# Kernel optimization log

Measured on AMD Instinct MI355X. Metric: run time of the kernel, lower is better.

Reference implementation:

```python
import jax, jax.numpy as jnp
import numpy as np

# HGIN_classifier: two relational-GIN layers with ReLU between.
# FastRGIN layer math (relational GIN, eps=0, single-linear MLP):
#   agg_r[i] = sum_{(j->i) with edge_type r} x[j]          (per-relation neighbor sum)
#   out[i]   = (1+eps) * x[i] @ W_self + sum_r agg_r[i] @ W_r + b

N = 100000      # nodes
E = 1600000     # edges (avg degree 16)
R = 2           # relations (follower / following)
DIN, DH, DOUT = 128, 256, 2
EPS = 0.0


def setup_inputs() -> dict:
    key = jax.random.key(0)
    ks = jax.random.split(key, 8)
    x = jax.random.normal(ks[0], (N, DIN), dtype=jnp.float32)
    edge_index = jax.random.randint(ks[1], (2, E), 0, N, dtype=jnp.int64)
    edge_type = jax.random.randint(ks[2], (E,), 0, R, dtype=jnp.int64)
    s1 = 1.0 / np.sqrt(DIN).astype(np.float32)
    s2 = 1.0 / np.sqrt(DH).astype(np.float32)
    w1_self = jax.random.normal(ks[3], (DIN, DH), jnp.float32) * s1
    w1_rel = jax.random.normal(ks[4], (R, DIN, DH), jnp.float32) * s1
    b1 = jnp.zeros((DH,), jnp.float32)
    w2_self = jax.random.normal(ks[5], (DH, DOUT), jnp.float32) * s2
    w2_rel = jax.random.normal(ks[6], (R, DH, DOUT), jnp.float32) * s2
    b2 = jnp.zeros((DOUT,), jnp.float32)
    return {"x": x, "edge_index": edge_index, "edge_type": edge_type,
            "w1_self": w1_self, "w1_rel": w1_rel, "b1": b1,
            "w2_self": w2_self, "w2_rel": w2_rel, "b2": b2}


def _rgin_layer(x, src, dst, etype, w_self, w_rel, b):
    n = x.shape[0]
    r = w_rel.shape[0]
    # fused (node, relation) segment id so one segment_sum handles all relations
    seg = dst * r + etype                                   # [E]
    agg = jax.ops.segment_sum(x[src], seg, num_segments=n * r)  # [N*R, d_in]
    agg = agg.reshape(n, r, -1)                              # [N, R, d_in]
    return (1.0 + EPS) * (x @ w_self) + jnp.einsum('nri,rio->no', agg, w_rel) + b


def reference(x, edge_index, edge_type, w1_self, w1_rel, b1, w2_self, w2_rel, b2):
    src, dst = edge_index[0], edge_index[1]
    h = jax.nn.relu(_rgin_layer(x, src, dst, edge_type, w1_self, w1_rel, b1))
    out = _rgin_layer(h, src, dst, edge_type, w2_self, w2_rel, b2)
    return out
```

## Files before the change

kernel.cpp:

```cpp
#include <hip/hip_runtime.h>


typedef _Float16 f16;
typedef _Float16 f16x2 __attribute__((ext_vector_type(2)));
typedef _Float16 f16x4 __attribute__((ext_vector_type(4)));
typedef _Float16 f16x8 __attribute__((ext_vector_type(8)));
typedef float    f32x4 __attribute__((ext_vector_type(4)));

constexpr int NN   = 100000;
constexpr int NR   = NN * 2;
constexpr int NB   = 512;
constexpr int BSH  = 9;
constexpr int CHUNK = 8192;

__global__ void zero_small(int* __restrict__ gcnt) {
  int t = threadIdx.x;
  if (t < NB) gcnt[t] = 0;
}

__global__ void bucketA(const int* __restrict__ dst, const int* __restrict__ et,
                        int* __restrict__ gcnt, int E) {
  __shared__ int h[NB];
  int t = threadIdx.x;
  for (int b = t; b < NB; b += 256) h[b] = 0;
  __syncthreads();
  int lo = blockIdx.x * CHUNK, hi = min(E, lo + CHUNK);
  for (int e = lo + t; e < hi; e += 256)
    atomicAdd(&h[(dst[e] * 2 + et[e]) >> BSH], 1);
  __syncthreads();
  for (int b = t; b < NB; b += 256) {
    int c = h[b];
    if (c) atomicAdd(&gcnt[b], c);
  }
}

__global__ void bscan(const int* __restrict__ gcnt, int* __restrict__ bstart,
                      int* __restrict__ gbase) {
  __shared__ int s[NB];
  int t = threadIdx.x;
  int v = gcnt[t];
  s[t] = v;
  __syncthreads();
  #pragma unroll
  for (int o = 1; o < NB; o <<= 1) {
    int u = (t >= o) ? s[t - o] : 0;
    __syncthreads();
    s[t] += u;
    __syncthreads();
  }
  bstart[t] = s[t] - v;
  gbase[t]  = s[t] - v;
  if (t == NB - 1) bstart[NB] = s[t];
}

__global__ void bucketB(const int* __restrict__ src, const int* __restrict__ dst,
                        const int* __restrict__ et, int* __restrict__ gbase,
                        int2* __restrict__ ebuf, int E) {
  __shared__ int h[NB], base[NB];
  int t = threadIdx.x;
  for (int b = t; b < NB; b += 256) h[b] = 0;
  __syncthreads();
  int lo = blockIdx.x * CHUNK, hi = min(E, lo + CHUNK);
  for (int e = lo + t; e < hi; e += 256)
    atomicAdd(&h[(dst[e] * 2 + et[e]) >> BSH], 1);
  __syncthreads();
  for (int b = t; b < NB; b += 256) {
    int c = h[b];
    base[b] = c ? atomicAdd(&gbase[b], c) : 0;
    h[b] = 0;
  }
  __syncthreads();
  for (int e = lo + t; e < hi; e += 256) {
    int seg = dst[e] * 2 + et[e];
    int b = seg >> BSH;
    int r = atomicAdd(&h[b], 1);
    ebuf[base[b] + r] = make_int2(src[e], seg);
  }
}

__global__ void bucketC(const int2* __restrict__ ebuf, const int* __restrict__ bstart,
                        int* __restrict__ off, int* __restrict__ srcs) {
  __shared__ int sh[NB], soff[NB], cnt[NB], tmp[256];
  int b = blockIdx.x, t = threadIdx.x;
  int lo = bstart[b], hi = bstart[b + 1];
  for (int s0 = t; s0 < NB; s0 += 256) { sh[s0] = 0; cnt[s0] = 0; }
  __syncthreads();
  for (int e = lo + t; e < hi; e += 256)
    atomicAdd(&sh[ebuf[e].y - (b << BSH)], 1);
  __syncthreads();
  int a0 = sh[2 * t], a1 = sh[2 * t + 1];
  tmp[t] = a0 + a1;
  __syncthreads();
  #pragma unroll
  for (int o = 1; o < 256; o <<= 1) {
    int u = (t >= o) ? tmp[t - o] : 0;
    __syncthreads();
    tmp[t] += u;
    __syncthreads();
  }
  int ex = tmp[t] - (a0 + a1);
  soff[2 * t] = ex;
  soff[2 * t + 1] = ex + a0;
  __syncthreads();
  int g0 = (b << BSH) + 2 * t;
  if (g0 <= NR)     off[g0]     = lo + soff[2 * t];
  if (g0 + 1 <= NR) off[g0 + 1] = lo + soff[2 * t + 1];
  for (int e = lo + t; e < hi; e += 256) {
    int2 p = ebuf[e];
    int s = p.y - (b << BSH);
    int r = atomicAdd(&cnt[s], 1);
    srcs[lo + soff[s] + r] = p.x;
  }
}

__global__ void cvt_x(const float4* __restrict__ xf, f16* __restrict__ xh, int n4) {
  int i = blockIdx.x * blockDim.x + threadIdx.x;
  if (i >= n4) return;
  float4 v = xf[i];
  f16x4 h;
  h.x = (f16)v.x; h.y = (f16)v.y; h.z = (f16)v.z; h.w = (f16)v.w;
  *(f16x4*)(xh + (size_t)i * 4) = h;
}

__global__ void cvt_w(const float* __restrict__ w1s, const float* __restrict__ w1r,
                      f16* __restrict__ w1t) {
  int id = blockIdx.x * blockDim.x + threadIdx.x;
  if (id >= 12 * 256 * 32) return;
  int ks = id >> 13, rem = id & 8191;
  int n = rem >> 5, ki = rem & 31;
  int k = ks * 32 + ki;
  float v = (k < 128) ? w1s[k * 256 + n] : w1r[(k - 128) * 256 + n];
  w1t[id] = (f16)v;
}

__global__ void aggregate(const f16* __restrict__ xh, const int* __restrict__ off,
                          const int* __restrict__ srcs, f16* __restrict__ aggh) {
  int w = (blockIdx.x * blockDim.x + threadIdx.x) >> 6;
  if (w >= NN) return;
  int lane = threadIdx.x & 63;
  int e0 = off[2 * w];
  int e1 = off[2 * w + 1];
  int e2 = off[2 * w + 2];
  float a0 = 0.f, a1 = 0.f, c0 = 0.f, c1 = 0.f;
  int e = e0;
  for (; e + 3 < e1; e += 4) {
    f16x2 v0 = *(const f16x2*)(xh + (long)srcs[e] * 128 + lane * 2);
    f16x2 v1 = *(const f16x2*)(xh + (long)srcs[e + 1] * 128 + lane * 2);
    f16x2 v2 = *(const f16x2*)(xh + (long)srcs[e + 2] * 128 + lane * 2);
    f16x2 v3 = *(const f16x2*)(xh + (long)srcs[e + 3] * 128 + lane * 2);
    a0 += (float)v0.x + (float)v1.x + (float)v2.x + (float)v3.x;
    a1 += (float)v0.y + (float)v1.y + (float)v2.y + (float)v3.y;
  }
  for (; e < e1; ++e) {
    f16x2 v = *(const f16x2*)(xh + (long)srcs[e] * 128 + lane * 2);
    a0 += (float)v.x; a1 += (float)v.y;
  }
  e = e1;
  for (; e + 3 < e2; e += 4) {
    f16x2 v0 = *(const f16x2*)(xh + (long)srcs[e] * 128 + lane * 2);
    f16x2 v1 = *(const f16x2*)(xh + (long)srcs[e + 1] * 128 + lane * 2);
    f16x2 v2 = *(const f16x2*)(xh + (long)srcs[e + 2] * 128 + lane * 2);
    f16x2 v3 = *(const f16x2*)(xh + (long)srcs[e + 3] * 128 + lane * 2);
    c0 += (float)v0.x + (float)v1.x + (float)v2.x + (float)v3.x;
    c1 += (float)v0.y + (float)v1.y + (float)v2.y + (float)v3.y;
  }
  for (; e < e2; ++e) {
    f16x2 v = *(const f16x2*)(xh + (long)srcs[e] * 128 + lane * 2);
    c0 += (float)v.x; c1 += (float)v.y;
  }
  f16* row = aggh + (long)w * 256;
  f16x2 o0; o0.x = (f16)a0; o0.y = (f16)a1;
  f16x2 o1; o1.x = (f16)c0; o1.y = (f16)c1;
  *(f16x2*)(row + lane * 2) = o0;
  *(f16x2*)(row + 128 + lane * 2) = o1;
}

__global__ __launch_bounds__(256) void gemm_mfma(
    const f16* __restrict__ xh, const f16* __restrict__ aggh,
    const f16* __restrict__ w1t,
    const float* __restrict__ b1, const float* __restrict__ w2s,
    const float* __restrict__ w2r, const float* __restrict__ b2,
    float* __restrict__ z2, float* __restrict__ out) {
  __shared__ float zbuf[4][64][6];
  const int t = threadIdx.x;
  const int lane = t & 63, wv = t >> 6;
  const int ml = lane & 15, quad = lane >> 4;
  const long rowBase = (long)blockIdx.x * 64;

  long rowc[4];
  #pragma unroll
  for (int mt = 0; mt < 4; ++mt) {
    long r = rowBase + mt * 16 + ml;
    rowc[mt] = r < NN ? r : (NN - 1);
  }
  const f16* bbase = w1t + (long)(wv * 64 + ml) * 32 + quad * 8;

  f32x4 acc[4][4];
  #pragma unroll
  for (int mt = 0; mt < 4; ++mt)
    #pragma unroll
    for (int nt = 0; nt < 4; ++nt) acc[mt][nt] = (f32x4)(0.f);

  #pragma unroll
  for (int ks = 0; ks < 12; ++ks) {
    f16x8 af[4], bf[4];
    #pragma unroll
    for (int mt = 0; mt < 4; ++mt) {
      const f16* ap = (ks < 4)
          ? (xh + rowc[mt] * 128 + ks * 32 + quad * 8)
          : (aggh + rowc[mt] * 256 + (ks - 4) * 32 + quad * 8);
      af[mt] = *(const f16x8*)ap;
    }
    #pragma unroll
    for (int nt = 0; nt < 4; ++nt)
      bf[nt] = *(const f16x8*)(bbase + (long)ks * 8192 + nt * 16 * 32);
    #pragma unroll
    for (int mt = 0; mt < 4; ++mt)
      #pragma unroll
      for (int nt = 0; nt < 4; ++nt)
        acc[mt][nt] = __builtin_amdgcn_mfma_f32_16x16x32_f16(af[mt], bf[nt],
                                                             acc[mt][nt], 0, 0, 0);
  }

  #pragma unroll
  for (int mt = 0; mt < 4; ++mt) {
    float z[4][6];
    #pragma unroll
    for (int rr = 0; rr < 4; ++rr)
      #pragma unroll
      for (int p = 0; p < 6; ++p) z[rr][p] = 0.f;
    #pragma unroll
    for (int nt = 0; nt < 4; ++nt) {
      int col = wv * 64 + nt * 16 + ml;
      float bb = b1[col];
      float wA = w2r[col * 2 + 0];
      float wB = w2r[col * 2 + 1];
      float wC = w2r[512 + col * 2 + 0];
      float wD = w2r[512 + col * 2 + 1];
      float wE = w2s[col * 2 + 0];
      float wF = w2s[col * 2 + 1];
      #pragma unroll
      for (int rr = 0; rr < 4; ++rr) {
        float h = acc[mt][nt][rr] + bb;
        h = h > 0.f ? h : 0.f;
        z[rr][0] = fmaf(h, wA, z[rr][0]);
        z[rr][1] = fmaf(h, wB, z[rr][1]);
        z[rr][2] = fmaf(h, wC, z[rr][2]);
        z[rr][3] = fmaf(h, wD, z[rr][3]);
        z[rr][4] = fmaf(h, wE, z[rr][4]);
        z[rr][5] = fmaf(h, wF, z[rr][5]);
      }
    }
    #pragma unroll
    for (int rr = 0; rr < 4; ++rr)
      #pragma unroll
      for (int p = 0; p < 6; ++p) {
        float v = z[rr][p];
        v += __shfl_xor(v, 1);
        v += __shfl_xor(v, 2);
        v += __shfl_xor(v, 4);
        v += __shfl_xor(v, 8);
        if (ml == 0) zbuf[wv][mt * 16 + quad * 4 + rr][p] = v;
      }
  }
  __syncthreads();
  for (int i = t; i < 384; i += 256) {
    int r = i / 6, p = i % 6;
    long grow = rowBase + r;
    if (grow < NN) {
      float v = zbuf[0][r][p] + zbuf[1][r][p] + zbuf[2][r][p] + zbuf[3][r][p];
      if (p < 4) z2[grow * 4 + p] = v;
      else       out[grow * 2 + (p - 4)] = v + b2[p - 4];
    }
  }
}

__global__ void gather2(const float* __restrict__ z2, const int* __restrict__ off,
                        const int* __restrict__ srcs, float* __restrict__ out) {
  int tid = blockIdx.x * blockDim.x + threadIdx.x;
  int n = tid >> 2;
  if (n >= NN) return;
  int sub = tid & 3;
  int e0 = off[2 * n];
  int e1 = off[2 * n + 1];
  int e2 = off[2 * n + 2];
  float o0 = 0.f, o1 = 0.f;
  for (int e = e0 + sub; e < e1; e += 4) {
    float2 v = *(const float2*)(z2 + (long)srcs[e] * 4);
    o0 += v.x; o1 += v.y;
  }
  for (int e = e1 + sub; e < e2; e += 4) {
    float2 v = *(const float2*)(z2 + (long)srcs[e] * 4 + 2);
    o0 += v.x; o1 += v.y;
  }
  o0 += __shfl_xor(o0, 1); o1 += __shfl_xor(o1, 1);
  o0 += __shfl_xor(o0, 2); o1 += __shfl_xor(o1, 2);
  if (sub == 0) {
    out[n * 2 + 0] += o0;
    out[n * 2 + 1] += o1;
  }
}

extern "C" void kernel_launch(void* const* d_in, const int* in_sizes, int n_in,
                              void* d_out, int out_size, void* d_ws, size_t ws_size,
                              hipStream_t stream) {
  const float* x   = (const float*)d_in[0];
  const int*   ei  = (const int*)d_in[1];
  const int*   et  = (const int*)d_in[2];
  const float* w1s = (const float*)d_in[3];
  const float* w1r = (const float*)d_in[4];
  const float* b1  = (const float*)d_in[5];
  const float* w2s = (const float*)d_in[6];
  const float* w2r = (const float*)d_in[7];
  const float* b2  = (const float*)d_in[8];
  float* out = (float*)d_out;
  const int E = in_sizes[2];
  const int* src = ei;
  const int* dst = ei + E;

  f16*   aggh = (f16*)d_ws;
  f16*   xh   = aggh + (size_t)NN * 256;
  f16*   w1t  = xh + (size_t)NN * 128;
  float* z2   = (float*)(w1t + 12 * 256 * 32);
  int2*  ebuf = (int2*)(z2 + (size_t)NN * 4);
  int*   srcs = (int*)(ebuf + E);
  int*   off  = srcs + E;
  int*   gcnt = off + NR + 1;
  int*   bstart = gcnt + NB;
  int*   gbase  = bstart + NB + 1;

  int nblk = (E + CHUNK - 1) / CHUNK;
  zero_small<<<1, 512, 0, stream>>>(gcnt);
  bucketA<<<nblk, 256, 0, stream>>>(dst, et, gcnt, E);
  bscan<<<1, 512, 0, stream>>>(gcnt, bstart, gbase);
  bucketB<<<nblk, 256, 0, stream>>>(src, dst, et, gbase, ebuf, E);
  bucketC<<<NB, 256, 0, stream>>>(ebuf, bstart, off, srcs);

  int n4 = NN * 128 / 4;
  cvt_x<<<(n4 + 255) / 256, 256, 0, stream>>>((const float4*)x, xh, n4);
  cvt_w<<<(12 * 256 * 32 + 255) / 256, 256, 0, stream>>>(w1s, w1r, w1t);

  aggregate<<<(NN * 64 + 255) / 256, 256, 0, stream>>>(xh, off, srcs, aggh);

  gemm_mfma<<<(NN + 63) / 64, 256, 0, stream>>>(xh, aggh, w1t, b1, w2s, w2r, b2,
                                                z2, out);

  gather2<<<(NN * 4 + 255) / 256, 256, 0, stream>>>(z2, off, srcs, out);
}
```

Before: 385.9 us.

## Fuse neighbor aggregation into layer-1 MFMA GEMM via shared-memory A tile

Removes the separate aggregate kernel and the aggh global buffer. Each GEMM block now stages its 64 rows of xh into padded LDS, runs the per-relation neighbor sums with one wave per node, writes them into the same LDS tile, and then feeds the MFMA loop from LDS. This avoids writing and re-reading the aggregated feature matrix through global memory. In exchange it uses about 50 KB of LDS per block, which limits occupancy, and the gather latency now sits inside the GEMM kernel with only 4 waves per block to hide it.

```diff
diff --git a/kernel.cpp b/kernel.cpp
--- a/kernel.cpp
+++ b/kernel.cpp
@@ -12,6 +12,7 @@
 constexpr int NB   = 512;
 constexpr int BSH  = 9;
 constexpr int CHUNK = 8192;
+constexpr int APAD = 392;
 
 __global__ void zero_small(int* __restrict__ gcnt) {
   int t = threadIdx.x;
@@ -133,68 +134,71 @@
   w1t[id] = (f16)v;
 }
 
-__global__ void aggregate(const f16* __restrict__ xh, const int* __restrict__ off,
-                          const int* __restrict__ srcs, f16* __restrict__ aggh) {
-  int w = (blockIdx.x * blockDim.x + threadIdx.x) >> 6;
-  if (w >= NN) return;
-  int lane = threadIdx.x & 63;
-  int e0 = off[2 * w];
-  int e1 = off[2 * w + 1];
-  int e2 = off[2 * w + 2];
-  float a0 = 0.f, a1 = 0.f, c0 = 0.f, c1 = 0.f;
-  int e = e0;
-  for (; e + 3 < e1; e += 4) {
-    f16x2 v0 = *(const f16x2*)(xh + (long)srcs[e] * 128 + lane * 2);
-    f16x2 v1 = *(const f16x2*)(xh + (long)srcs[e + 1] * 128 + lane * 2);
-    f16x2 v2 = *(const f16x2*)(xh + (long)srcs[e + 2] * 128 + lane * 2);
-    f16x2 v3 = *(const f16x2*)(xh + (long)srcs[e + 3] * 128 + lane * 2);
-    a0 += (float)v0.x + (float)v1.x + (float)v2.x + (float)v3.x;
-    a1 += (float)v0.y + (float)v1.y + (float)v2.y + (float)v3.y;
-  }
-  for (; e < e1; ++e) {
-    f16x2 v = *(const f16x2*)(xh + (long)srcs[e] * 128 + lane * 2);
-    a0 += (float)v.x; a1 += (float)v.y;
-  }
-  e = e1;
-  for (; e + 3 < e2; e += 4) {
-    f16x2 v0 = *(const f16x2*)(xh + (long)srcs[e] * 128 + lane * 2);
-    f16x2 v1 = *(const f16x2*)(xh + (long)srcs[e + 1] * 128 + lane * 2);
-    f16x2 v2 = *(const f16x2*)(xh + (long)srcs[e + 2] * 128 + lane * 2);
-    f16x2 v3 = *(const f16x2*)(xh + (long)srcs[e + 3] * 128 + lane * 2);
-    c0 += (float)v0.x + (float)v1.x + (float)v2.x + (float)v3.x;
-    c1 += (float)v0.y + (float)v1.y + (float)v2.y + (float)v3.y;
-  }
-  for (; e < e2; ++e) {
-    f16x2 v = *(const f16x2*)(xh + (long)srcs[e] * 128 + lane * 2);
-    c0 += (float)v.x; c1 += (float)v.y;
-  }
-  f16* row = aggh + (long)w * 256;
-  f16x2 o0; o0.x = (f16)a0; o0.y = (f16)a1;
-  f16x2 o1; o1.x = (f16)c0; o1.y = (f16)c1;
-  *(f16x2*)(row + lane * 2) = o0;
-  *(f16x2*)(row + 128 + lane * 2) = o1;
-}
-
-__global__ __launch_bounds__(256) void gemm_mfma(
-    const f16* __restrict__ xh, const f16* __restrict__ aggh,
-    const f16* __restrict__ w1t,
+__global__ __launch_bounds__(256) void gemm_fused(
+    const f16* __restrict__ xh, const int* __restrict__ off,
+    const int* __restrict__ srcs, const f16* __restrict__ w1t,
     const float* __restrict__ b1, const float* __restrict__ w2s,
     const float* __restrict__ w2r, const float* __restrict__ b2,
     float* __restrict__ z2, float* __restrict__ out) {
-  __shared__ float zbuf[4][64][6];
+  __shared__ __align__(16) f16 Ash[64 * APAD];
+  float (*zbuf)[64][6] = (float (*)[64][6])(void*)Ash;
   const int t = threadIdx.x;
   const int lane = t & 63, wv = t >> 6;
   const int ml = lane & 15, quad = lane >> 4;
   const long rowBase = (long)blockIdx.x * 64;
 
-  long rowc[4];
-  #pragma unroll
-  for (int mt = 0; mt < 4; ++mt) {
-    long r = rowBase + mt * 16 + ml;
-    rowc[mt] = r < NN ? r : (NN - 1);
-  }
+  #pragma unroll
+  for (int j = 0; j < 4; ++j) {
+    int chunkId = t * 4 + j;
+    int r = chunkId >> 4, c = chunkId & 15;
+    long grow = rowBase + r;
+    uint4 v = make_uint4(0, 0, 0, 0);
+    if (grow < NN) v = *(const uint4*)(xh + grow * 128 + c * 8);
+    *(uint4*)&Ash[r * APAD + c * 8] = v;
+  }
+
+  for (int w = wv; w < 64; w += 4) {
+    long node = rowBase + w;
+    float a0 = 0.f, a1 = 0.f, c0 = 0.f, c1 = 0.f;
+    if (node < NN) {
+      int e0 = off[2 * node], e1 = off[2 * node + 1], e2 = off[2 * node + 2];
+      int e = e0;
+      for (; e + 3 < e1; e += 4) {
+        int s0 = srcs[e], s1 = srcs[e + 1], s2 = srcs[e + 2], s3 = srcs[e + 3];
+        f16x2 v0 = *(const f16x2*)(xh + (long)s0 * 128 + lane * 2);
+        f16x2 v1 = *(const f16x2*)(xh + (long)s1 * 128 + lane * 2);
+        f16x2 v2 = *(const f16x2*)(xh + (long)s2 * 128 + lane * 2);
+        f16x2 v3 = *(const f16x2*)(xh + (long)s3 * 128 + lane * 2);
+        a0 += (float)v0.x + (float)v1.x + (float)v2.x + (float)v3.x;
+        a1 += (float)v0.y + (float)v1.y + (float)v2.y + (float)v3.y;
+      }
+      for (; e < e1; ++e) {
+        f16x2 v = *(const f16x2*)(xh + (long)srcs[e] * 128 + lane * 2);
+        a0 += (float)v.x; a1 += (float)v.y;
+      }
+      e = e1;
+      for (; e + 3 < e2; e += 4) {
+        int s0 = srcs[e], s1 = srcs[e + 1], s2 = srcs[e + 2], s3 = srcs[e + 3];
+        f16x2 v0 = *(const f16x2*)(xh + (long)s0 * 128 + lane * 2);
+        f16x2 v1 = *(const f16x2*)(xh + (long)s1 * 128 + lane * 2);
+        f16x2 v2 = *(const f16x2*)(xh + (long)s2 * 128 + lane * 2);
+        f16x2 v3 = *(const f16x2*)(xh + (long)s3 * 128 + lane * 2);
+        c0 += (float)v0.x + (float)v1.x + (float)v2.x + (float)v3.x;
+        c1 += (float)v0.y + (float)v1.y + (float)v2.y + (float)v3.y;
+      }
+      for (; e < e2; ++e) {
+        f16x2 v = *(const f16x2*)(xh + (long)srcs[e] * 128 + lane * 2);
+        c0 += (float)v.x; c1 += (float)v.y;
+      }
+    }
+    f16x2 o0; o0.x = (f16)a0; o0.y = (f16)a1;
+    f16x2 o1; o1.x = (f16)c0; o1.y = (f16)c1;
+    *(f16x2*)&Ash[w * APAD + 128 + lane * 2] = o0;
+    *(f16x2*)&Ash[w * APAD + 256 + lane * 2] = o1;
+  }
+  __syncthreads();
+
   const f16* bbase = w1t + (long)(wv * 64 + ml) * 32 + quad * 8;
-
   f32x4 acc[4][4];
   #pragma unroll
   for (int mt = 0; mt < 4; ++mt)
@@ -205,12 +209,8 @@
   for (int ks = 0; ks < 12; ++ks) {
     f16x8 af[4], bf[4];
     #pragma unroll
-    for (int mt = 0; mt < 4; ++mt) {
-      const f16* ap = (ks < 4)
-          ? (xh + rowc[mt] * 128 + ks * 32 + quad * 8)
-          : (aggh + rowc[mt] * 256 + (ks - 4) * 32 + quad * 8);
-      af[mt] = *(const f16x8*)ap;
-    }
+    for (int mt = 0; mt < 4; ++mt)
+      af[mt] = *(const f16x8*)&Ash[(mt * 16 + ml) * APAD + ks * 32 + quad * 8];
     #pragma unroll
     for (int nt = 0; nt < 4; ++nt)
       bf[nt] = *(const f16x8*)(bbase + (long)ks * 8192 + nt * 16 * 32);
@@ -221,6 +221,7 @@
         acc[mt][nt] = __builtin_amdgcn_mfma_f32_16x16x32_f16(af[mt], bf[nt],
                                                              acc[mt][nt], 0, 0, 0);
   }
+  __syncthreads();
 
   #pragma unroll
   for (int mt = 0; mt < 4; ++mt) {
@@ -318,8 +319,7 @@
   const int* src = ei;
   const int* dst = ei + E;
 
-  f16*   aggh = (f16*)d_ws;
-  f16*   xh   = aggh + (size_t)NN * 256;
+  f16*   xh   = (f16*)d_ws;
   f16*   w1t  = xh + (size_t)NN * 128;
   float* z2   = (float*)(w1t + 12 * 256 * 32);
   int2*  ebuf = (int2*)(z2 + (size_t)NN * 4);
@@ -340,10 +340,8 @@
   cvt_x<<<(n4 + 255) / 256, 256, 0, stream>>>((const float4*)x, xh, n4);
   cvt_w<<<(12 * 256 * 32 + 255) / 256, 256, 0, stream>>>(w1s, w1r, w1t);
 
-  aggregate<<<(NN * 64 + 255) / 256, 256, 0, stream>>>(xh, off, srcs, aggh);
-
-  gemm_mfma<<<(NN + 63) / 64, 256, 0, stream>>>(xh, aggh, w1t, b1, w2s, w2r, b2,
-                                                z2, out);
+  gemm_fused<<<(NN + 63) / 64, 256, 0, stream>>>(xh, off, srcs, w1t,
+                                                 b1, w2s, w2r, b2, z2, out);
 
   gather2<<<(NN * 4 + 255) / 256, 256, 0, stream>>>(z2, off, srcs, out);
 }
```

Result: slower. 522.1 us (+35.3%).
